# Performance work log

Measured on AMD Instinct MI355X. Metric: run time of the kernel, lower is better.

## Reference

```python
import jax, jax.numpy as jnp
import numpy as np

SEARCH_RANGE = 4  # max displacement -> 9x9 = 81 offsets
LEAKY_ALPHA = 0.1


def setup_inputs() -> dict:
    key = jax.random.key(0)
    k1, k2, k3 = jax.random.split(key, 3)
    B, H, W, C = 16, 96, 96, 128
    prv = jax.random.normal(k1, (B, H, W, C), dtype=jnp.float32)
    nxt = jax.random.normal(k2, (B, H, W, C), dtype=jnp.float32)
    # Conv2D(filters=2, kernel_size=3, padding='same'); in_channels = 81 + 2*C = 337
    fan_in, fan_out = 3 * 3 * 337, 3 * 3 * 2
    limit = np.sqrt(6.0 / (fan_in + fan_out))  # glorot_uniform
    conv_w = jax.random.uniform(k3, (3, 3, 337, 2), minval=-limit, maxval=limit, dtype=jnp.float32)
    conv_b = jnp.zeros((2,), dtype=jnp.float32)
    return {"prv": prv, "nxt": nxt, "conv_w": conv_w, "conv_b": conv_b}


def _cost_volume(prv, nxt):
    sr = SEARCH_RANGE
    padded = jnp.pad(nxt, ((0, 0), (sr, sr), (sr, sr), (0, 0)))
    H, W = prv.shape[1], prv.shape[2]
    n = 2 * sr + 1
    # 81 fixed static offsets: slice + per-pixel channel-mean correlation
    costs = [
        jnp.mean(prv * jax.lax.slice(padded, (0, y, x, 0), (padded.shape[0], y + H, x + W, padded.shape[3])), axis=-1)
        for y in range(n) for x in range(n)
    ]
    cost = jnp.stack(costs, axis=-1)  # [B, H, W, 81]
    return jnp.where(cost >= 0, cost, LEAKY_ALPHA * cost)  # leaky_relu(0.1)


def reference(prv, nxt, conv_w, conv_b):
    cost = _cost_volume(prv, nxt)
    feat = jnp.concatenate([cost, prv, nxt], axis=-1)  # [B, H, W, 337]
    out = jax.lax.conv_general_dilated(
        feat, conv_w, window_strides=(1, 1), padding='SAME',
        dimension_numbers=('NHWC', 'HWIO', 'NHWC'))
    return out + conv_b  # [B, H, W, 2]
```

## Files before the change

kernel.cpp:

```cpp
#include <hip/hip_runtime.h>
#include <hip/hip_fp16.h>

#define HH 96
#define WW 96
#define CC 128

typedef float f32x4 __attribute__((ext_vector_type(4)));
typedef short short8 __attribute__((ext_vector_type(8)));
typedef _Float16 f16x8 __attribute__((ext_vector_type(8)));

union U32H2 { unsigned int u; __half2 h; };
__device__ __forceinline__ unsigned int pack2(float x, float y){ U32H2 t; t.h=__floats2half2_rn(x,y); return t.u; }

__device__ __forceinline__ unsigned short f2bf(float x){
  unsigned int u = __float_as_uint(x);
  return (unsigned short)((u + 0x7FFFu + ((u >> 16) & 1u)) >> 16);
}
__device__ __forceinline__ unsigned int pkbf(float a, float b){
  return (unsigned)f2bf(a) | ((unsigned)f2bf(b) << 16);
}

union U4S8 { uint4 q; short8 s; };
union U4H8 { uint4 q; f16x8 h; };

__global__ __launch_bounds__(512, 4) void k_cost_mfma(const float* __restrict__ prv,
                                                      const float* __restrict__ nxt,
                                                      __half* __restrict__ cost) {
  const int x0 = blockIdx.x * 16;
  const int y0 = blockIdx.y * 8;
  const int b  = blockIdx.z;
  const int tid = threadIdx.x;
  const int w = tid >> 6, l = tid & 63;
  const int lm = l & 15, lq = l >> 4;
  const int y = y0 + w;

  __shared__ uint4 ntile[2][1568];
  __shared__ uint4 ptile[2][512];

  f32x4 acc[9][2];
#pragma unroll
  for (int dy = 0; dy < 9; ++dy) {
    acc[dy][0] = (f32x4){0.f,0.f,0.f,0.f};
    acc[dy][1] = (f32x4){0.f,0.f,0.f,0.f};
  }

  const int sr = tid >> 5, sp = tid & 31;
  const int gr = y0 - 4 + sr, gc = x0 - 4 + sp;
  const bool nok = (sp < 24) && ((unsigned)gr < HH) && ((unsigned)gc < WW);
  const float* nrow = &nxt[((size_t)(b*HH + gr)*WW + gc)*CC];
  const int sq = (tid >> 4) & 3, spp = tid & 15;
  const float* prow = &prv[((size_t)(b*HH + y0 + (tid >> 6))*WW + x0 + spp)*CC + sq*8];

  auto stage = [&](int ks, int buf){
    float4 f[8];
#pragma unroll
    for (int j = 0; j < 8; ++j) f[j] = make_float4(0.f,0.f,0.f,0.f);
    if (nok) {
      const float* src = nrow + ks*32;
#pragma unroll
      for (int j = 0; j < 8; ++j) f[j] = *(const float4*)(src + j*4);
    }
    const float4 g0 = *(const float4*)(prow + ks*32);
    const float4 g1 = *(const float4*)(prow + ks*32 + 4);
    if (sp < 24) {
#pragma unroll
      for (int kq = 0; kq < 4; ++kq) {
        uint4 d;
        d.x = pkbf(f[2*kq].x,   f[2*kq].y);
        d.y = pkbf(f[2*kq].z,   f[2*kq].w);
        d.z = pkbf(f[2*kq+1].x, f[2*kq+1].y);
        d.w = pkbf(f[2*kq+1].z, f[2*kq+1].w);
        ntile[buf][(sr*4 + kq)*24 + sp] = d;
      }
    }
    uint4 pd;
    pd.x = pkbf(g0.x, g0.y); pd.y = pkbf(g0.z, g0.w);
    pd.z = pkbf(g1.x, g1.y); pd.w = pkbf(g1.z, g1.w);
    ptile[buf][tid] = pd;
  };

  stage(0, 0);

#pragma unroll 1
  for (int ks = 0; ks < 4; ++ks) {
    __syncthreads();
    if (ks < 3) stage(ks + 1, (ks + 1) & 1);

    const int cur = ks & 1;
    U4S8 af;
    af.q = ptile[cur][(w*4 + lq)*16 + lm];
#pragma unroll
    for (int dy = 0; dy < 9; ++dy) {
      const int sb = ((w + dy)*4 + lq)*24;
      U4S8 b0, b1;
      b0.q = ntile[cur][sb + lm];
      b1.q = ntile[cur][sb + 16 + lm];
      acc[dy][0] = __builtin_amdgcn_mfma_f32_16x16x32_bf16(af.s, b0.s, acc[dy][0], 0, 0, 0);
      acc[dy][1] = __builtin_amdgcn_mfma_f32_16x16x32_bf16(af.s, b1.s, acc[dy][1], 0, 0, 0);
    }
  }

#pragma unroll
  for (int t = 0; t < 2; ++t) {
#pragma unroll
    for (int reg = 0; reg < 4; ++reg) {
      const int m  = lq*4 + reg;
      const int od = t*16 + lm - m;
      if (od >= 0 && od <= 8) {
        __half* bp = &cost[((size_t)(b*HH + y)*WW + x0 + m)*96 + od];
#pragma unroll
        for (int dy = 0; dy < 9; ++dy) {
          float v = acc[dy][t][reg] * 0.0078125f;
          v = (v >= 0.f) ? v : 0.1f * v;
          bp[dy*9] = __float2half(v);
        }
      }
    }
  }
}

__global__ __launch_bounds__(512) void k_conv_gemm(const float* __restrict__ prv,
                                                   const float* __restrict__ nxt,
                                                   const __half* __restrict__ cost,
                                                   const float* __restrict__ cw,
                                                   const float* __restrict__ cb,
                                                   float* __restrict__ out) {
  const int tw0 = blockIdx.x*16, th0 = blockIdx.y*16, b = blockIdx.z;
  const int tid = threadIdx.x;
  const int w = tid >> 6, l = tid & 63;
  const int lm = l & 15, lq = l >> 4;

  __shared__ __align__(16) char smem[49408];
  uint4*        feat16 = (uint4*)smem;
  float*        Gf     = (float*)smem;
  float2*       Gf2    = (float2*)smem;
  uint4*        B2     = (uint4*)(smem + 26880);
  __half*       B2h    = (__half*)(smem + 26880);

#pragma unroll 1
  for (int i = tid; i < 5632; i += 512) ((unsigned int*)B2)[i] = 0u;
#pragma unroll 1
  for (int i = tid; i < 240; i += 512) ((unsigned int*)smem)[6480 + i] = 0u;
#pragma unroll 1
  for (int i = tid; i < 352*18; i += 512) {
    const int ci = i / 18, j = i - 18*ci;
    if (ci >= 81 && ci < 96) continue;
    const int wci = (ci < 81) ? ci : ci - 15;
    const int tap = j >> 1, n = j & 1;
    const float v = cw[(tap*337 + wci)*2 + n];
    const int kk = ci & 31;
    B2h[((((ci >> 5)*4 + (kk >> 3))*32) + j)*8 + (kk & 7)] = __float2half(v);
  }

  f32x4 acc[3][2];
#pragma unroll
  for (int i = 0; i < 3; ++i) { acc[i][0] = (f32x4){0,0,0,0}; acc[i][1] = (f32x4){0,0,0,0}; }

#pragma unroll 1
  for (int kc = 0; kc < 11; ++kc) {
    __syncthreads();
#pragma unroll 1
    for (int i = tid; i < 648; i += 512) {
      const int px = i >> 1, half = i & 1;
      const int hr = px / 18, hc = px - 18*hr;
      const int gr = th0 - 1 + hr, gc = tw0 - 1 + hc;
      uint4 d0 = make_uint4(0,0,0,0), d1 = make_uint4(0,0,0,0);
      if ((unsigned)gr < HH && (unsigned)gc < WW) {
        const size_t pixi = (size_t)(b*HH + gr)*WW + gc;
        if (kc < 3) {
          const uint4* cs = (const uint4*)&cost[pixi*96 + kc*32 + half*16];
          d0 = cs[0]; d1 = cs[1];
        } else {
          const float* src = (kc < 7) ? prv : nxt;
          const int c0 = ((kc < 7) ? (kc-3) : (kc-7))*32 + half*16;
          const float4 f0 = *(const float4*)&src[pixi*128 + c0];
          const float4 f1 = *(const float4*)&src[pixi*128 + c0 + 4];
          const float4 f2 = *(const float4*)&src[pixi*128 + c0 + 8];
          const float4 f3 = *(const float4*)&src[pixi*128 + c0 + 12];
          d0 = make_uint4(pack2(f0.x,f0.y), pack2(f0.z,f0.w), pack2(f1.x,f1.y), pack2(f1.z,f1.w));
          d1 = make_uint4(pack2(f2.x,f2.y), pack2(f2.z,f2.w), pack2(f3.x,f3.y), pack2(f3.z,f3.w));
        }
      }
      feat16[5*px + 2*half]     = d0;
      feat16[5*px + 2*half + 1] = d1;
    }
    __syncthreads();

    U4H8 bf0, bf1;
    bf0.q = B2[(kc*4 + lq)*32 + lm];
    bf1.q = B2[(kc*4 + lq)*32 + 16 + lm];
#pragma unroll
    for (int i = 0; i < 3; ++i) {
      const int mf = w + 8*i;
      if (mf < 21) {
        U4H8 af;
        af.q = feat16[5*(16*mf + lm) + lq];
        acc[i][0] = __builtin_amdgcn_mfma_f32_16x16x32_f16(af.h, bf0.h, acc[i][0], 0, 0, 0);
        acc[i][1] = __builtin_amdgcn_mfma_f32_16x16x32_f16(af.h, bf1.h, acc[i][1], 0, 0, 0);
      }
    }
  }
  __syncthreads();

#pragma unroll
  for (int i = 0; i < 3; ++i) {
    const int mf = w + 8*i;
    if (mf >= 21) continue;
#pragma unroll
    for (int r = 0; r < 4; ++r) {
      const int px = 16*mf + lq*4 + r;
      if (px < 324) {
        Gf[px*20 + lm] = acc[i][0][r];
        if (lm < 2) Gf[px*20 + 16 + lm] = acc[i][1][r];
      }
    }
  }
  __syncthreads();

  if (tid < 512) {
    const int px = tid >> 1, n = tid & 1;
    const int ty = px >> 4, tx = px & 15;
    float s = cb[n];
#pragma unroll
    for (int p = 0; p < 9; ++p) {
      const int dy = p / 3, dx = p - 3*dy;
      const int hp = (ty + dy)*18 + (tx + dx);
      const float2 g = Gf2[hp*10 + p];
      s += n ? g.y : g.x;
    }
    out[((size_t)(b*HH + th0 + ty)*WW + (tw0 + tx))*2 + n] = s;
  }
}

extern "C" void kernel_launch(void* const* d_in, const int* in_sizes, int n_in,
                              void* d_out, int out_size, void* d_ws, size_t ws_size,
                              hipStream_t stream) {
  const float* prv = (const float*)d_in[0];
  const float* nxt = (const float*)d_in[1];
  const float* cw  = (const float*)d_in[2];
  const float* cb  = (const float*)d_in[3];
  __half* cost = (__half*)d_ws;

  k_cost_mfma<<<dim3(6, 12, 16), dim3(512), 0, stream>>>(prv, nxt, cost);
  k_conv_gemm<<<dim3(6, 6, 16), dim3(512), 0, stream>>>(prv, nxt, cost, cw, cb, (float*)d_out);
}
```

Before: 128.2 us.

## Split cost-volume dy range across wave pairs with 4-row tiles

Each cost block now covers 4 output rows instead of 8, and each row is handled by two waves that split the 9 vertical displacements 5/4. This halves per-wave accumulator registers and doubles the grid, aiming for more occupancy and parallelism. The trade-off is that the nxt halo now takes a larger share of each tile (12 rows for 4 outputs rather than 16 for 8), so more global loads and bf16 conversions are repeated. Staging is also split by role: threads below 384 load nxt and the remaining 128 threads load prv.

Result: faster. 118.5 us (-7.6%).

```diff
diff --git a/kernel.cpp b/kernel.cpp
--- a/kernel.cpp
+++ b/kernel.cpp
@@ -22,61 +22,87 @@
 
 union U4S8 { uint4 q; short8 s; };
 union U4H8 { uint4 q; f16x8 h; };
+
+template<int DY0, int NDY>
+static __device__ __forceinline__ void cost_mma(const uint4* __restrict__ nt,
+                                                int yr, int lq, int lm,
+                                                short8 a, f32x4 (&acc)[5][2]) {
+#pragma unroll
+  for (int d = 0; d < NDY; ++d) {
+    const int sb = ((yr + DY0 + d)*4 + lq)*24;
+    U4S8 b0, b1;
+    b0.q = nt[sb + lm];
+    b1.q = nt[sb + 16 + lm];
+    acc[d][0] = __builtin_amdgcn_mfma_f32_16x16x32_bf16(a, b0.s, acc[d][0], 0, 0, 0);
+    acc[d][1] = __builtin_amdgcn_mfma_f32_16x16x32_bf16(a, b1.s, acc[d][1], 0, 0, 0);
+  }
+}
 
 __global__ __launch_bounds__(512, 4) void k_cost_mfma(const float* __restrict__ prv,
                                                       const float* __restrict__ nxt,
                                                       __half* __restrict__ cost) {
   const int x0 = blockIdx.x * 16;
-  const int y0 = blockIdx.y * 8;
+  const int y0 = blockIdx.y * 4;
   const int b  = blockIdx.z;
   const int tid = threadIdx.x;
   const int w = tid >> 6, l = tid & 63;
   const int lm = l & 15, lq = l >> 4;
-  const int y = y0 + w;
-
-  __shared__ uint4 ntile[2][1568];
-  __shared__ uint4 ptile[2][512];
-
-  f32x4 acc[9][2];
-#pragma unroll
-  for (int dy = 0; dy < 9; ++dy) {
-    acc[dy][0] = (f32x4){0.f,0.f,0.f,0.f};
-    acc[dy][1] = (f32x4){0.f,0.f,0.f,0.f};
+  const int yr = w >> 1, hf = w & 1;
+  const int y = y0 + yr;
+
+  __shared__ uint4 ntile[2][1280];
+  __shared__ uint4 ptile[2][256];
+
+  f32x4 acc[5][2];
+#pragma unroll
+  for (int d = 0; d < 5; ++d) {
+    acc[d][0] = (f32x4){0.f,0.f,0.f,0.f};
+    acc[d][1] = (f32x4){0.f,0.f,0.f,0.f};
   }
 
   const int sr = tid >> 5, sp = tid & 31;
   const int gr = y0 - 4 + sr, gc = x0 - 4 + sp;
-  const bool nok = (sp < 24) && ((unsigned)gr < HH) && ((unsigned)gc < WW);
-  const float* nrow = &nxt[((size_t)(b*HH + gr)*WW + gc)*CC];
-  const int sq = (tid >> 4) & 3, spp = tid & 15;
-  const float* prow = &prv[((size_t)(b*HH + y0 + (tid >> 6))*WW + x0 + spp)*CC + sq*8];
+  const bool nok = (tid < 384) && (sp < 24) && ((unsigned)gr < HH) && ((unsigned)gc < WW);
+  const float* nrow = &nxt[((size_t)(b*HH + ((unsigned)gr < HH ? gr : 0))*WW
+                            + ((unsigned)gc < WW ? gc : 0))*CC];
+  const int pidx = (tid >= 384) ? (tid - 384) : 0;
+  const int prow_i = pidx >> 5, pq0 = (pidx >> 4) & 1, ppx = pidx & 15;
+  const float* prow = &prv[((size_t)(b*HH + y0 + prow_i)*WW + x0 + ppx)*CC];
 
   auto stage = [&](int ks, int buf){
-    float4 f[8];
-#pragma unroll
-    for (int j = 0; j < 8; ++j) f[j] = make_float4(0.f,0.f,0.f,0.f);
-    if (nok) {
-      const float* src = nrow + ks*32;
-#pragma unroll
-      for (int j = 0; j < 8; ++j) f[j] = *(const float4*)(src + j*4);
-    }
-    const float4 g0 = *(const float4*)(prow + ks*32);
-    const float4 g1 = *(const float4*)(prow + ks*32 + 4);
-    if (sp < 24) {
-#pragma unroll
-      for (int kq = 0; kq < 4; ++kq) {
-        uint4 d;
-        d.x = pkbf(f[2*kq].x,   f[2*kq].y);
-        d.y = pkbf(f[2*kq].z,   f[2*kq].w);
-        d.z = pkbf(f[2*kq+1].x, f[2*kq+1].y);
-        d.w = pkbf(f[2*kq+1].z, f[2*kq+1].w);
-        ntile[buf][(sr*4 + kq)*24 + sp] = d;
-      }
-    }
-    uint4 pd;
-    pd.x = pkbf(g0.x, g0.y); pd.y = pkbf(g0.z, g0.w);
-    pd.z = pkbf(g1.x, g1.y); pd.w = pkbf(g1.z, g1.w);
-    ptile[buf][tid] = pd;
+    if (tid < 384) {
+      float4 f[8];
+#pragma unroll
+      for (int j = 0; j < 8; ++j) f[j] = make_float4(0.f,0.f,0.f,0.f);
+      if (nok) {
+        const float* src = nrow + ks*32;
+#pragma unroll
+        for (int j = 0; j < 8; ++j) f[j] = *(const float4*)(src + j*4);
+      }
+      if (sp < 24) {
+#pragma unroll
+        for (int kq = 0; kq < 4; ++kq) {
+          uint4 d;
+          d.x = pkbf(f[2*kq].x,   f[2*kq].y);
+          d.y = pkbf(f[2*kq].z,   f[2*kq].w);
+          d.z = pkbf(f[2*kq+1].x, f[2*kq+1].y);
+          d.w = pkbf(f[2*kq+1].z, f[2*kq+1].w);
+          ntile[buf][(sr*4 + kq)*24 + sp] = d;
+        }
+      }
+    } else {
+#pragma unroll
+      for (int qq = 0; qq < 2; ++qq) {
+        const int q = pq0 + 2*qq;
+        const float* s = prow + ks*32 + q*8;
+        const float4 a0 = *(const float4*)s;
+        const float4 a1 = *(const float4*)(s + 4);
+        uint4 pd;
+        pd.x = pkbf(a0.x, a0.y); pd.y = pkbf(a0.z, a0.w);
+        pd.z = pkbf(a1.x, a1.y); pd.w = pkbf(a1.z, a1.w);
+        ptile[buf][(prow_i*4 + q)*16 + ppx] = pd;
+      }
+    }
   };
 
   stage(0, 0);
@@ -88,18 +114,13 @@
 
     const int cur = ks & 1;
     U4S8 af;
-    af.q = ptile[cur][(w*4 + lq)*16 + lm];
-#pragma unroll
-    for (int dy = 0; dy < 9; ++dy) {
-      const int sb = ((w + dy)*4 + lq)*24;
-      U4S8 b0, b1;
-      b0.q = ntile[cur][sb + lm];
-      b1.q = ntile[cur][sb + 16 + lm];
-      acc[dy][0] = __builtin_amdgcn_mfma_f32_16x16x32_bf16(af.s, b0.s, acc[dy][0], 0, 0, 0);
-      acc[dy][1] = __builtin_amdgcn_mfma_f32_16x16x32_bf16(af.s, b1.s, acc[dy][1], 0, 0, 0);
-    }
-  }
-
+    af.q = ptile[cur][(yr*4 + lq)*16 + lm];
+    const uint4* nt = ntile[cur];
+    if (hf == 0) cost_mma<0,5>(nt, yr, lq, lm, af.s, acc);
+    else         cost_mma<5,4>(nt, yr, lq, lm, af.s, acc);
+  }
+
+  const int DY0 = hf ? 5 : 0, NDY = hf ? 4 : 5;
 #pragma unroll
   for (int t = 0; t < 2; ++t) {
 #pragma unroll
@@ -107,12 +128,14 @@
       const int m  = lq*4 + reg;
       const int od = t*16 + lm - m;
       if (od >= 0 && od <= 8) {
-        __half* bp = &cost[((size_t)(b*HH + y)*WW + x0 + m)*96 + od];
-#pragma unroll
-        for (int dy = 0; dy < 9; ++dy) {
-          float v = acc[dy][t][reg] * 0.0078125f;
-          v = (v >= 0.f) ? v : 0.1f * v;
-          bp[dy*9] = __float2half(v);
+        __half* bp = &cost[((size_t)(b*HH + y)*WW + x0 + m)*96 + DY0*9 + od];
+#pragma unroll
+        for (int d = 0; d < 5; ++d) {
+          if (d < NDY) {
+            float v = acc[d][t][reg] * 0.0078125f;
+            v = (v >= 0.f) ? v : 0.1f * v;
+            bp[d*9] = __float2half(v);
+          }
         }
       }
     }
@@ -241,6 +264,6 @@
   const float* cb  = (const float*)d_in[3];
   __half* cost = (__half*)d_ws;
 
-  k_cost_mfma<<<dim3(6, 12, 16), dim3(512), 0, stream>>>(prv, nxt, cost);
+  k_cost_mfma<<<dim3(6, 24, 16), dim3(512), 0, stream>>>(prv, nxt, cost);
   k_conv_gemm<<<dim3(6, 6, 16), dim3(512), 0, stream>>>(prv, nxt, cost, cw, cb, (float*)d_out);
 }
```

## Split cost-volume blocks to two rows with three dy-groups per warp

Applied to the files above, without the earlier changes.

The cost-volume kernel now gives each block 2 output rows instead of 8 and uses 6 warps, each handling one row and a group of 3 vertical displacements. The grid grows fourfold and per-thread accumulators drop from 18 to 6 vectors. Fewer registers and more, smaller blocks are meant to raise occupancy and give a better spread across CUs. The cost is extra halo traffic, since each block reloads a 10-row nxt tile for only 2 output rows, and the staging work is now split unevenly between threads.

Result: slower. 142.4 us (+11.0%).

```diff
diff --git a/kernel.cpp b/kernel.cpp
--- a/kernel.cpp
+++ b/kernel.cpp
@@ -23,46 +23,48 @@
 union U4S8 { uint4 q; short8 s; };
 union U4H8 { uint4 q; f16x8 h; };
 
-__global__ __launch_bounds__(512, 4) void k_cost_mfma(const float* __restrict__ prv,
+__global__ __launch_bounds__(384, 6) void k_cost_mfma(const float* __restrict__ prv,
                                                       const float* __restrict__ nxt,
                                                       __half* __restrict__ cost) {
   const int x0 = blockIdx.x * 16;
-  const int y0 = blockIdx.y * 8;
+  const int y0 = blockIdx.y * 2;
   const int b  = blockIdx.z;
   const int tid = threadIdx.x;
   const int w = tid >> 6, l = tid & 63;
   const int lm = l & 15, lq = l >> 4;
-  const int y = y0 + w;
-
-  __shared__ uint4 ntile[2][1568];
-  __shared__ uint4 ptile[2][512];
-
-  f32x4 acc[9][2];
-#pragma unroll
-  for (int dy = 0; dy < 9; ++dy) {
-    acc[dy][0] = (f32x4){0.f,0.f,0.f,0.f};
-    acc[dy][1] = (f32x4){0.f,0.f,0.f,0.f};
-  }
-
-  const int sr = tid >> 5, sp = tid & 31;
-  const int gr = y0 - 4 + sr, gc = x0 - 4 + sp;
-  const bool nok = (sp < 24) && ((unsigned)gr < HH) && ((unsigned)gc < WW);
-  const float* nrow = &nxt[((size_t)(b*HH + gr)*WW + gc)*CC];
-  const int sq = (tid >> 4) & 3, spp = tid & 15;
-  const float* prow = &prv[((size_t)(b*HH + y0 + (tid >> 6))*WW + x0 + spp)*CC + sq*8];
+  const int yr = w & 1, dg = w >> 1;
+  const int y = y0 + yr;
+
+  __shared__ uint4 ntile[2][976];
+  __shared__ uint4 ptile[2][128];
+
+  f32x4 acc[3][2];
+#pragma unroll
+  for (int d = 0; d < 3; ++d) {
+    acc[d][0] = (f32x4){0.f,0.f,0.f,0.f};
+    acc[d][1] = (f32x4){0.f,0.f,0.f,0.f};
+  }
+
+  const int srow = tid / 24, scol = tid - 24*srow;
+  const int gr = y0 - 4 + srow, gc = x0 - 4 + scol;
+  const bool nok = (tid < 240) && ((unsigned)gr < HH) && ((unsigned)gc < WW);
+  const float* nrow = &nxt[((size_t)(b*HH + ((unsigned)gr < HH ? gr : 0))*WW
+                            + ((unsigned)gc < WW ? gc : 0))*CC];
+  const bool pok = (tid >= 240) && (tid < 368);
+  const int pidx = pok ? (tid - 240) : 0;
+  const int prow_i = pidx >> 6, pq = (pidx >> 4) & 3, ppx = pidx & 15;
+  const float* prow = &prv[((size_t)(b*HH + y0 + prow_i)*WW + x0 + ppx)*CC + pq*8];
 
   auto stage = [&](int ks, int buf){
-    float4 f[8];
-#pragma unroll
-    for (int j = 0; j < 8; ++j) f[j] = make_float4(0.f,0.f,0.f,0.f);
-    if (nok) {
-      const float* src = nrow + ks*32;
-#pragma unroll
-      for (int j = 0; j < 8; ++j) f[j] = *(const float4*)(src + j*4);
-    }
-    const float4 g0 = *(const float4*)(prow + ks*32);
-    const float4 g1 = *(const float4*)(prow + ks*32 + 4);
-    if (sp < 24) {
+    if (tid < 240) {
+      float4 f[8];
+#pragma unroll
+      for (int j = 0; j < 8; ++j) f[j] = make_float4(0.f,0.f,0.f,0.f);
+      if (nok) {
+        const float* src = nrow + ks*32;
+#pragma unroll
+        for (int j = 0; j < 8; ++j) f[j] = *(const float4*)(src + j*4);
+      }
 #pragma unroll
       for (int kq = 0; kq < 4; ++kq) {
         uint4 d;
@@ -70,13 +72,17 @@
         d.y = pkbf(f[2*kq].z,   f[2*kq].w);
         d.z = pkbf(f[2*kq+1].x, f[2*kq+1].y);
         d.w = pkbf(f[2*kq+1].z, f[2*kq+1].w);
-        ntile[buf][(sr*4 + kq)*24 + sp] = d;
-      }
-    }
-    uint4 pd;
-    pd.x = pkbf(g0.x, g0.y); pd.y = pkbf(g0.z, g0.w);
-    pd.z = pkbf(g1.x, g1.y); pd.w = pkbf(g1.z, g1.w);
-    ptile[buf][tid] = pd;
+        ntile[buf][(srow*4 + kq)*24 + scol] = d;
+      }
+    } else if (pok) {
+      const float* s = prow + ks*32;
+      const float4 a0 = *(const float4*)s;
+      const float4 a1 = *(const float4*)(s + 4);
+      uint4 pd;
+      pd.x = pkbf(a0.x, a0.y); pd.y = pkbf(a0.z, a0.w);
+      pd.z = pkbf(a1.x, a1.y); pd.w = pkbf(a1.z, a1.w);
+      ptile[buf][(prow_i*4 + pq)*16 + ppx] = pd;
+    }
   };
 
   stage(0, 0);
@@ -88,18 +94,19 @@
 
     const int cur = ks & 1;
     U4S8 af;
-    af.q = ptile[cur][(w*4 + lq)*16 + lm];
-#pragma unroll
-    for (int dy = 0; dy < 9; ++dy) {
-      const int sb = ((w + dy)*4 + lq)*24;
+    af.q = ptile[cur][(yr*4 + lq)*16 + lm];
+#pragma unroll
+    for (int d = 0; d < 3; ++d) {
+      const int sb = ((yr + dg*3 + d)*4 + lq)*24;
       U4S8 b0, b1;
       b0.q = ntile[cur][sb + lm];
       b1.q = ntile[cur][sb + 16 + lm];
-      acc[dy][0] = __builtin_amdgcn_mfma_f32_16x16x32_bf16(af.s, b0.s, acc[dy][0], 0, 0, 0);
-      acc[dy][1] = __builtin_amdgcn_mfma_f32_16x16x32_bf16(af.s, b1.s, acc[dy][1], 0, 0, 0);
-    }
-  }
-
+      acc[d][0] = __builtin_amdgcn_mfma_f32_16x16x32_bf16(af.s, b0.s, acc[d][0], 0, 0, 0);
+      acc[d][1] = __builtin_amdgcn_mfma_f32_16x16x32_bf16(af.s, b1.s, acc[d][1], 0, 0, 0);
+    }
+  }
+
+  const int ch0 = dg*27;
 #pragma unroll
   for (int t = 0; t < 2; ++t) {
 #pragma unroll
@@ -107,12 +114,12 @@
       const int m  = lq*4 + reg;
       const int od = t*16 + lm - m;
       if (od >= 0 && od <= 8) {
-        __half* bp = &cost[((size_t)(b*HH + y)*WW + x0 + m)*96 + od];
-#pragma unroll
-        for (int dy = 0; dy < 9; ++dy) {
-          float v = acc[dy][t][reg] * 0.0078125f;
+        __half* bp = &cost[((size_t)(b*HH + y)*WW + x0 + m)*96 + ch0 + od];
+#pragma unroll
+        for (int d = 0; d < 3; ++d) {
+          float v = acc[d][t][reg] * 0.0078125f;
           v = (v >= 0.f) ? v : 0.1f * v;
-          bp[dy*9] = __float2half(v);
+          bp[d*9] = __float2half(v);
         }
       }
     }
@@ -241,6 +248,6 @@
   const float* cb  = (const float*)d_in[3];
   __half* cost = (__half*)d_ws;
 
-  k_cost_mfma<<<dim3(6, 12, 16), dim3(512), 0, stream>>>(prv, nxt, cost);
+  k_cost_mfma<<<dim3(6, 48, 16), dim3(384), 0, stream>>>(prv, nxt, cost);
   k_conv_gemm<<<dim3(6, 6, 16), dim3(512), 0, stream>>>(prv, nxt, cost, cw, cb, (float*)d_out);
 }
```
